# Kernel tuning notes

Measured on AMD Instinct MI355X. Metric: run time of the kernel, lower is better.

The kernel has to match this reference:

```python
import jax, jax.numpy as jnp
import numpy as np

B, S, D = 1, 4096, 768
H = 12
HD = D // H  # 64


def setup_inputs() -> dict:
    key = jax.random.key(0)
    ks = jax.random.split(key, 6)
    sc = 1.0 / np.sqrt(D)
    return {
        "x": jax.random.normal(ks[0], (B, S, D), dtype=jnp.float32),
        "wq": jax.random.normal(ks[1], (D, D), dtype=jnp.float32) * sc,
        "wk": jax.random.normal(ks[2], (D, D), dtype=jnp.float32) * sc,
        "wv": jax.random.normal(ks[3], (D, D), dtype=jnp.float32) * sc,
        "wo": jax.random.normal(ks[4], (D, D), dtype=jnp.float32) * sc,
        "bo": jax.random.normal(ks[5], (D,), dtype=jnp.float32) * 0.02,
    }


def reference(x, wq, wk, wv, wo, bo):
    b, n, _ = x.shape
    # projections (torch Linear: x @ W.T; here weights stored as (d_in, d_out))
    q = (x @ wq).reshape(b, n, H, HD).transpose(0, 2, 1, 3)  # b h n d
    k = (x @ wk).reshape(b, n, H, HD).transpose(0, 2, 1, 3)
    v = (x @ wv).reshape(b, n, H, HD).transpose(0, 2, 1, 3)
    scores = jnp.einsum("bhqd,bhkd->bhqk", q, k)
    causal = jnp.tril(jnp.ones((n, n), dtype=bool))  # True = keep
    scores = jnp.where(causal, scores, -jnp.inf)
    weights = jax.nn.softmax(scores / np.sqrt(HD), axis=-1)
    ctx = jnp.einsum("bhqk,bhkd->bhqd", weights, v)
    ctx = ctx.transpose(0, 2, 1, 3).reshape(b, n, D)
    return ctx @ wo + bo
```

## Files before the change

kernel.cpp:

```cpp
#include <hip/hip_runtime.h>


typedef short bf16x8 __attribute__((ext_vector_type(8)));
typedef float f32x4 __attribute__((ext_vector_type(4)));
typedef unsigned short u16;

static constexpr int S_LEN = 4096;
static constexpr int DIM   = 768;
static constexpr int NH    = 12;
static constexpr float QSCALE = 0.125f * 1.44269504088896340736f;

__device__ inline u16 f2bf(float f) {
  union { float f; unsigned int u; } v; v.f = f;
  unsigned int r = v.u + 0x7FFFu + ((v.u >> 16) & 1u);
  return (u16)(r >> 16);
}

__device__ inline void gload_lds16(const u16* g, u16* s) {
  __builtin_amdgcn_global_load_lds(
      (const __attribute__((address_space(1))) unsigned int*)g,
      (__attribute__((address_space(3))) unsigned int*)s, 16, 0, 0);
}

__device__ inline bf16x8 packP(f32x4 sA, f32x4 sB, float& ls) {
  const float p0 = __builtin_amdgcn_exp2f(sA[0]);
  const float p1 = __builtin_amdgcn_exp2f(sA[1]);
  const float p2 = __builtin_amdgcn_exp2f(sA[2]);
  const float p3 = __builtin_amdgcn_exp2f(sA[3]);
  const float r0 = __builtin_amdgcn_exp2f(sB[0]);
  const float r1 = __builtin_amdgcn_exp2f(sB[1]);
  const float r2 = __builtin_amdgcn_exp2f(sB[2]);
  const float r3 = __builtin_amdgcn_exp2f(sB[3]);
  ls += (p0 + p1 + p2 + p3) + (r0 + r1 + r2 + r3);
  unsigned a0, a1, b0, b1;
  asm("v_cvt_pk_bf16_f32 %0, %1, %2" : "=v"(a0) : "v"(p0), "v"(p1));
  asm("v_cvt_pk_bf16_f32 %0, %1, %2" : "=v"(a1) : "v"(p2), "v"(p3));
  asm("v_cvt_pk_bf16_f32 %0, %1, %2" : "=v"(b0) : "v"(r0), "v"(r1));
  asm("v_cvt_pk_bf16_f32 %0, %1, %2" : "=v"(b1) : "v"(r2), "v"(r3));
  asm("v_permlane32_swap_b32 %0, %1" : "+v"(a0), "+v"(b0));
  asm("v_permlane16_swap_b32 %0, %1" : "+v"(a0), "+v"(b0));
  asm("v_permlane32_swap_b32 %0, %1" : "+v"(a1), "+v"(b1));
  asm("v_permlane16_swap_b32 %0, %1" : "+v"(a1), "+v"(b1));
  union { unsigned u[4]; bf16x8 v; } U;
  U.u[0] = a0; U.u[1] = a1; U.u[2] = b0; U.u[3] = b1;
  return U.v;
}

__device__ inline bf16x8 packPmask(f32x4 sA, f32x4 sB, float& ls,
                                   int kvb, int quad, int qg) {
  float p0 = __builtin_amdgcn_exp2f(sA[0]);
  float p1 = __builtin_amdgcn_exp2f(sA[1]);
  float p2 = __builtin_amdgcn_exp2f(sA[2]);
  float p3 = __builtin_amdgcn_exp2f(sA[3]);
  float r0 = __builtin_amdgcn_exp2f(sB[0]);
  float r1 = __builtin_amdgcn_exp2f(sB[1]);
  float r2 = __builtin_amdgcn_exp2f(sB[2]);
  float r3 = __builtin_amdgcn_exp2f(sB[3]);
  const int k0 = kvb + quad * 4;
  if (k0 + 0 > qg)  p0 = 0.f;
  if (k0 + 1 > qg)  p1 = 0.f;
  if (k0 + 2 > qg)  p2 = 0.f;
  if (k0 + 3 > qg)  p3 = 0.f;
  if (k0 + 16 > qg) r0 = 0.f;
  if (k0 + 17 > qg) r1 = 0.f;
  if (k0 + 18 > qg) r2 = 0.f;
  if (k0 + 19 > qg) r3 = 0.f;
  ls += (p0 + p1 + p2 + p3) + (r0 + r1 + r2 + r3);
  unsigned a0, a1, b0, b1;
  asm("v_cvt_pk_bf16_f32 %0, %1, %2" : "=v"(a0) : "v"(p0), "v"(p1));
  asm("v_cvt_pk_bf16_f32 %0, %1, %2" : "=v"(a1) : "v"(p2), "v"(p3));
  asm("v_cvt_pk_bf16_f32 %0, %1, %2" : "=v"(b0) : "v"(r0), "v"(r1));
  asm("v_cvt_pk_bf16_f32 %0, %1, %2" : "=v"(b1) : "v"(r2), "v"(r3));
  asm("v_permlane32_swap_b32 %0, %1" : "+v"(a0), "+v"(b0));
  asm("v_permlane16_swap_b32 %0, %1" : "+v"(a0), "+v"(b0));
  asm("v_permlane32_swap_b32 %0, %1" : "+v"(a1), "+v"(b1));
  asm("v_permlane16_swap_b32 %0, %1" : "+v"(a1), "+v"(b1));
  union { unsigned u[4]; bf16x8 v; } U;
  U.u[0] = a0; U.u[1] = a1; U.u[2] = b0; U.u[3] = b1;
  return U.v;
}

__global__ __launch_bounds__(256)
void prep_kernel(const float* __restrict__ x, const float* __restrict__ w0,
                 const float* __restrict__ w1, const float* __restrict__ w2,
                 const float* __restrict__ w3, u16* __restrict__ xb,
                 u16* __restrict__ t0, u16* __restrict__ t1,
                 u16* __restrict__ t2, u16* __restrict__ t3) {
  if (blockIdx.z == 4) {
    const size_t n = (size_t)S_LEN * DIM;
    const int id = blockIdx.y * 12 + blockIdx.x;
    const size_t stride = (size_t)144 * 256 * 8;
    for (size_t i = ((size_t)id * 256 + threadIdx.x) * 8; i < n; i += stride) {
      const float4 a = *(const float4*)(x + i);
      const float4 b = *(const float4*)(x + i + 4);
      bf16x8 o;
      o[0] = (short)f2bf(a.x); o[1] = (short)f2bf(a.y);
      o[2] = (short)f2bf(a.z); o[3] = (short)f2bf(a.w);
      o[4] = (short)f2bf(b.x); o[5] = (short)f2bf(b.y);
      o[6] = (short)f2bf(b.z); o[7] = (short)f2bf(b.w);
      *(bf16x8*)(xb + i) = o;
    }
    return;
  }
  __shared__ float T[64][65];
  const float* src; u16* dst;
  switch (blockIdx.z) {
    case 0: src = w0; dst = t0; break;
    case 1: src = w1; dst = t1; break;
    case 2: src = w2; dst = t2; break;
    default: src = w3; dst = t3; break;
  }
  const int k0 = blockIdx.y * 64, n0 = blockIdx.x * 64;
  const int r = threadIdx.x >> 2, c0 = (threadIdx.x & 3) * 16;
#pragma unroll
  for (int i = 0; i < 4; ++i) {
    const float4 v = *(const float4*)(src + (size_t)(k0 + r) * DIM + n0 + c0 + i * 4);
    T[r][c0 + i * 4 + 0] = v.x;
    T[r][c0 + i * 4 + 1] = v.y;
    T[r][c0 + i * 4 + 2] = v.z;
    T[r][c0 + i * 4 + 3] = v.w;
  }
  __syncthreads();
  bf16x8 o0, o1;
#pragma unroll
  for (int i = 0; i < 8; ++i) {
    o0[i] = (short)f2bf(T[c0 + i][r]);
    o1[i] = (short)f2bf(T[c0 + 8 + i][r]);
  }
  *(bf16x8*)(dst + (size_t)(n0 + r) * DIM + k0 + c0) = o0;
  *(bf16x8*)(dst + (size_t)(n0 + r) * DIM + k0 + c0 + 8) = o1;
}

template <int MODE>
__global__ __launch_bounds__(256)
void mfma_gemm_kernel(const u16* __restrict__ A, const u16* __restrict__ Bq,
                      const u16* __restrict__ Bk, const u16* __restrict__ Bv,
                      const float* __restrict__ bias, u16* __restrict__ Qb,
                      u16* __restrict__ Kb, u16* __restrict__ VT,
                      float* __restrict__ Out) {
  constexpr int MT = (MODE == 0) ? 4 : 2;
  constexpr int BM = MT * 32;
  __shared__ __align__(16) u16 Al[BM * 64];
  __shared__ __align__(16) u16 Bl[96 * 64];

  const int tid  = threadIdx.x;
  const int wv   = tid >> 6;
  const int lane = tid & 63;
  const int quad = lane >> 4;
  const int l16  = lane & 15;
  const int wr = wv >> 1, wc = wv & 1;
  const int m0 = blockIdx.y * BM;
  const int n0 = blockIdx.x * 96;

  int wi = 0, nb = n0;
  const u16* BT = Bq;
  if (MODE == 0) {
    wi = n0 / DIM;
    nb = n0 - wi * DIM;
    BT = (wi == 0) ? Bq : (wi == 1) ? Bk : Bv;
  }

  const int sr8 = lane >> 3;
  const int sc  = ((lane & 7) ^ sr8) * 8;
  const int key = l16 & 7;

  const bool swp = (MODE == 1) || (wi < 2);

  f32x4 acc[MT][3] = {};

  for (int k0 = 0; k0 < DIM; k0 += 64) {
    __syncthreads();
#pragma unroll
    for (int j = 0; j < MT; ++j)
      gload_lds16(A + (size_t)(m0 + wv * (BM / 4) + j * 8 + sr8) * DIM + k0 + sc,
                  &Al[(wv * (BM / 4) + j * 8) * 64]);
#pragma unroll
    for (int j = 0; j < 3; ++j)
      gload_lds16(BT + (size_t)(nb + wv * 24 + j * 8 + sr8) * DIM + k0 + sc,
                  &Bl[(wv * 24 + j * 8) * 64]);
    __syncthreads();

#pragma unroll
    for (int kh = 0; kh < 2; ++kh) {
      const int cb = kh * 4;
      bf16x8 af[MT], bfr[3];
#pragma unroll
      for (int mt = 0; mt < MT; ++mt) {
        const int row = wr * (BM / 2) + mt * 16 + l16;
        af[mt] = *(const bf16x8*)&Al[row * 64 + ((cb + quad) ^ key) * 8];
      }
#pragma unroll
      for (int nt = 0; nt < 3; ++nt) {
        const int row = wc * 48 + nt * 16 + l16;
        bfr[nt] = *(const bf16x8*)&Bl[row * 64 + ((cb + quad) ^ key) * 8];
      }
      if (swp) {
#pragma unroll
        for (int mt = 0; mt < MT; ++mt)
#pragma unroll
          for (int nt = 0; nt < 3; ++nt)
            acc[mt][nt] = __builtin_amdgcn_mfma_f32_16x16x32_bf16(
                bfr[nt], af[mt], acc[mt][nt], 0, 0, 0);
      } else {
#pragma unroll
        for (int mt = 0; mt < MT; ++mt)
#pragma unroll
          for (int nt = 0; nt < 3; ++nt)
            acc[mt][nt] = __builtin_amdgcn_mfma_f32_16x16x32_bf16(
                af[mt], bfr[nt], acc[mt][nt], 0, 0, 0);
      }
    }
  }

  if (MODE == 0 && wi >= 2) {
#pragma unroll
    for (int mt = 0; mt < MT; ++mt) {
#pragma unroll
      for (int nt = 0; nt < 3; ++nt) {
        const int row  = m0 + wr * (BM / 2) + mt * 16 + quad * 4;
        const int ncol = nb + wc * 48 + nt * 16 + l16;
        u16 pk[4];
#pragma unroll
        for (int r = 0; r < 4; ++r) pk[r] = f2bf(acc[mt][nt][r]);
        unsigned long long v;
        __builtin_memcpy(&v, pk, 8);
        *(unsigned long long*)(VT + (size_t)ncol * S_LEN + row) = v;
      }
    }
  } else if (MODE == 0) {
    u16* dst = (wi == 0) ? Qb : Kb;
    const float sc_out = (wi == 0) ? QSCALE : 1.0f;
#pragma unroll
    for (int mt = 0; mt < MT; ++mt) {
#pragma unroll
      for (int nt = 0; nt < 3; ++nt) {
        const int row = m0 + wr * (BM / 2) + mt * 16 + l16;
        const int ncb = nb + wc * 48 + nt * 16 + quad * 4;
        u16 pk[4];
#pragma unroll
        for (int r = 0; r < 4; ++r) pk[r] = f2bf(acc[mt][nt][r] * sc_out);
        unsigned long long v;
        __builtin_memcpy(&v, pk, 8);
        *(unsigned long long*)(dst + (size_t)row * DIM + ncb) = v;
      }
    }
  } else {
#pragma unroll
    for (int mt = 0; mt < MT; ++mt) {
#pragma unroll
      for (int nt = 0; nt < 3; ++nt) {
        const int row = m0 + wr * (BM / 2) + mt * 16 + l16;
        const int ncb = n0 + wc * 48 + nt * 16 + quad * 4;
        const float4 b4 = *(const float4*)(bias + ncb);
        float4 ov;
        ov.x = acc[mt][nt][0] + b4.x;
        ov.y = acc[mt][nt][1] + b4.y;
        ov.z = acc[mt][nt][2] + b4.z;
        ov.w = acc[mt][nt][3] + b4.w;
        *(float4*)(Out + (size_t)row * DIM + ncb) = ov;
      }
    }
  }
}

__global__ __launch_bounds__(256, 4)
void attn_mfma_kernel(const u16* __restrict__ Qb, const u16* __restrict__ Kb,
                      const u16* __restrict__ VTb, u16* __restrict__ ctx) {
  __shared__ __align__(16) u16 KVl[128 * 64 + 64 * 128];
  u16* const Kl = KVl;
  u16* const Vl = KVl + 128 * 64;

  const int tid  = threadIdx.x;
  const int w    = tid >> 6;
  const int lane = tid & 63;
  const int quad = lane >> 4;
  const int l16  = lane & 15;
  const int key  = l16 & 7;

  const int id = blockIdx.x;
  const int to = id / 12;
  const int h  = id - to * 12;
  const int qt = 127 - to;
  const int q0 = qt * 32;

  const int sr8  = lane >> 3;
  const int scK  = ((lane & 7) ^ sr8) * 8;
  const int sr16 = lane >> 4;

  bf16x8 aq00, aq01, aq10, aq11;
  {
    const u16* qp0 = Qb + (size_t)(q0 + l16) * DIM + h * 64 + quad * 8;
    aq00 = *(const bf16x8*)(qp0);
    aq01 = *(const bf16x8*)(qp0 + 32);
    const u16* qp1 = Qb + (size_t)(q0 + 16 + l16) * DIM + h * 64 + quad * 8;
    aq10 = *(const bf16x8*)(qp1);
    aq11 = *(const bf16x8*)(qp1 + 32);
  }

  f32x4 o00 = {}, o01 = {}, o02 = {}, o03 = {};
  f32x4 o10 = {}, o11 = {}, o12 = {}, o13 = {};
  float ls0 = 0.f, ls1 = 0.f;
  const int qg0 = q0 + l16;
  const int qg1 = q0 + 16 + l16;

  const int niter = qt / 4 + 1;

#pragma unroll 1
  for (int i = 0; i < niter; ++i) {
    const int k0g = i * 128;
    asm volatile("s_waitcnt lgkmcnt(0)" ::: "memory");
    __builtin_amdgcn_s_barrier();

#pragma unroll
    for (int jj = 0; jj < 4; ++jj)
      gload_lds16(Kb + (size_t)(k0g + w * 32 + jj * 8 + sr8) * DIM + h * 64 + scK,
                  &Kl[(w * 32 + jj * 8) * 64]);
#pragma unroll
    for (int jj = 0; jj < 4; ++jj) {
      const int vrow = w * 16 + jj * 4 + sr16;
      const int vcol = (l16 ^ (vrow & 7)) * 8;
      gload_lds16(VTb + (size_t)(h * 64 + vrow) * S_LEN + k0g + vcol,
                  &Vl[(w * 16 + jj * 4) * 128]);
    }
    asm volatile("s_waitcnt vmcnt(4)" ::: "memory");
    __builtin_amdgcn_s_barrier();

    const int g = 4 * i + w;
    const bool act = g <= qt;
    bf16x8 pa0v, pa1v;
    if (act) {
      __builtin_amdgcn_s_setprio(1);
      const int rA = (w * 32 + l16) * 64;
      const int rB = (w * 32 + 16 + l16) * 64;
      const bf16x8 bk00 = *(const bf16x8*)&Kl[rA + (quad ^ key) * 8];
      const bf16x8 bk01 = *(const bf16x8*)&Kl[rA + ((quad ^ 4) ^ key) * 8];
      const bf16x8 bk10 = *(const bf16x8*)&Kl[rB + (quad ^ key) * 8];
      const bf16x8 bk11 = *(const bf16x8*)&Kl[rB + ((quad ^ 4) ^ key) * 8];
      const f32x4 Z = {0.f, 0.f, 0.f, 0.f};
      f32x4 sA = __builtin_amdgcn_mfma_f32_16x16x32_bf16(bk00, aq00, Z, 0, 0, 0);
      sA = __builtin_amdgcn_mfma_f32_16x16x32_bf16(bk01, aq01, sA, 0, 0, 0);
      f32x4 sB = __builtin_amdgcn_mfma_f32_16x16x32_bf16(bk10, aq00, Z, 0, 0, 0);
      sB = __builtin_amdgcn_mfma_f32_16x16x32_bf16(bk11, aq01, sB, 0, 0, 0);
      f32x4 sC = __builtin_amdgcn_mfma_f32_16x16x32_bf16(bk00, aq10, Z, 0, 0, 0);
      sC = __builtin_amdgcn_mfma_f32_16x16x32_bf16(bk01, aq11, sC, 0, 0, 0);
      f32x4 sD = __builtin_amdgcn_mfma_f32_16x16x32_bf16(bk10, aq10, Z, 0, 0, 0);
      sD = __builtin_amdgcn_mfma_f32_16x16x32_bf16(bk11, aq11, sD, 0, 0, 0);

      if (g == qt) {
        const int kvb = k0g + w * 32;
        pa0v = packPmask(sA, sB, ls0, kvb, quad, qg0);
        pa1v = packPmask(sC, sD, ls1, kvb, quad, qg1);
      } else {
        pa0v = packP(sA, sB, ls0);
        pa1v = packP(sC, sD, ls1);
      }
    }

    asm volatile("s_waitcnt vmcnt(0)" ::: "memory");
    __builtin_amdgcn_s_barrier();

    if (act) {
      const int cc = ((w * 4 + quad) ^ key) * 8;
      const bf16x8 vb0 = *(const bf16x8*)&Vl[(l16) * 128 + cc];
      o00 = __builtin_amdgcn_mfma_f32_16x16x32_bf16(pa0v, vb0, o00, 0, 0, 0);
      o10 = __builtin_amdgcn_mfma_f32_16x16x32_bf16(pa1v, vb0, o10, 0, 0, 0);
      const bf16x8 vb1 = *(const bf16x8*)&Vl[(16 + l16) * 128 + cc];
      o01 = __builtin_amdgcn_mfma_f32_16x16x32_bf16(pa0v, vb1, o01, 0, 0, 0);
      o11 = __builtin_amdgcn_mfma_f32_16x16x32_bf16(pa1v, vb1, o11, 0, 0, 0);
      const bf16x8 vb2 = *(const bf16x8*)&Vl[(32 + l16) * 128 + cc];
      o02 = __builtin_amdgcn_mfma_f32_16x16x32_bf16(pa0v, vb2, o02, 0, 0, 0);
      o12 = __builtin_amdgcn_mfma_f32_16x16x32_bf16(pa1v, vb2, o12, 0, 0, 0);
      const bf16x8 vb3 = *(const bf16x8*)&Vl[(48 + l16) * 128 + cc];
      o03 = __builtin_amdgcn_mfma_f32_16x16x32_bf16(pa0v, vb3, o03, 0, 0, 0);
      o13 = __builtin_amdgcn_mfma_f32_16x16x32_bf16(pa1v, vb3, o13, 0, 0, 0);
      __builtin_amdgcn_s_setprio(0);
    }
  }

  __syncthreads();
  float* Obuf  = (float*)KVl;
  float* lbufF = Obuf + 5120;
  const int bme = (w * 64 + lane) * 20;

  *(f32x4*)&Obuf[bme + 0]  = o00;
  *(f32x4*)&Obuf[bme + 4]  = o01;
  *(f32x4*)&Obuf[bme + 8]  = o02;
  *(f32x4*)&Obuf[bme + 12] = o03;
  lbufF[w * 64 + lane] = ls0;
  __syncthreads();
  if (w == 0) {
#pragma unroll
    for (int wq = 1; wq < 4; ++wq) {
      const int bp = (wq * 64 + lane) * 20;
      o00 += *(const f32x4*)&Obuf[bp + 0];
      o01 += *(const f32x4*)&Obuf[bp + 4];
      o02 += *(const f32x4*)&Obuf[bp + 8];
      o03 += *(const f32x4*)&Obuf[bp + 12];
      ls0 += lbufF[wq * 64 + lane];
    }
  }
  __syncthreads();

  *(f32x4*)&Obuf[bme + 0]  = o10;
  *(f32x4*)&Obuf[bme + 4]  = o11;
  *(f32x4*)&Obuf[bme + 8]  = o12;
  *(f32x4*)&Obuf[bme + 12] = o13;
  lbufF[w * 64 + lane] = ls1;
  __syncthreads();
  if (w == 1) {
#pragma unroll
    for (int wq = 0; wq < 4; ++wq) {
      if (wq == 1) continue;
      const int bp = (wq * 64 + lane) * 20;
      o10 += *(const f32x4*)&Obuf[bp + 0];
      o11 += *(const f32x4*)&Obuf[bp + 4];
      o12 += *(const f32x4*)&Obuf[bp + 8];
      o13 += *(const f32x4*)&Obuf[bp + 12];
      ls1 += lbufF[wq * 64 + lane];
    }
  }

  if (w == 0) {
    float L = ls0;
    L += __shfl_xor(L, 16);
    L += __shfl_xor(L, 32);
#pragma unroll
    for (int r = 0; r < 4; ++r) {
      const float inv = 1.f / __shfl(L, quad * 4 + r);
      const int row = q0 + quad * 4 + r;
      u16* cp = ctx + (size_t)row * DIM + h * 64 + l16;
      cp[0]  = f2bf(o00[r] * inv);
      cp[16] = f2bf(o01[r] * inv);
      cp[32] = f2bf(o02[r] * inv);
      cp[48] = f2bf(o03[r] * inv);
    }
  } else if (w == 1) {
    float L = ls1;
    L += __shfl_xor(L, 16);
    L += __shfl_xor(L, 32);
#pragma unroll
    for (int r = 0; r < 4; ++r) {
      const float inv = 1.f / __shfl(L, quad * 4 + r);
      const int row = q0 + 16 + quad * 4 + r;
      u16* cp = ctx + (size_t)row * DIM + h * 64 + l16;
      cp[0]  = f2bf(o10[r] * inv);
      cp[16] = f2bf(o11[r] * inv);
      cp[32] = f2bf(o12[r] * inv);
      cp[48] = f2bf(o13[r] * inv);
    }
  }
}

extern "C" void kernel_launch(void* const* d_in, const int* in_sizes, int n_in,
                              void* d_out, int out_size, void* d_ws,
                              size_t ws_size, hipStream_t stream) {
  const float* x  = (const float*)d_in[0];
  const float* wq = (const float*)d_in[1];
  const float* wk = (const float*)d_in[2];
  const float* wv = (const float*)d_in[3];
  const float* wo = (const float*)d_in[4];
  const float* bo = (const float*)d_in[5];

  const size_t n_x = (size_t)S_LEN * DIM;
  const size_t n_w = (size_t)DIM * DIM;
  u16* xb  = (u16*)d_ws;
  u16* wtq = xb + n_x;
  u16* wtk = wtq + n_w;
  u16* wtv = wtk + n_w;
  u16* wto = wtv + n_w;
  u16* Qb  = wto + n_w;
  u16* Kb  = Qb + n_x;
  u16* VTb = Kb + n_x;
  u16* ctx = VTb + n_x;

  prep_kernel<<<dim3(12, 12, 5), 256, 0, stream>>>(
      x, wq, wk, wv, wo, xb, wtq, wtk, wtv, wto);

  mfma_gemm_kernel<0><<<dim3(24, 32), 256, 0, stream>>>(
      xb, wtq, wtk, wtv, nullptr, Qb, Kb, VTb, nullptr);

  attn_mfma_kernel<<<dim3(1536), 256, 0, stream>>>(Qb, Kb, VTb, ctx);

  mfma_gemm_kernel<1><<<dim3(8, 64), 256, 0, stream>>>(
      ctx, wto, nullptr, nullptr, bo, nullptr, nullptr, nullptr, (float*)d_out);
}
```

Measured before the change: 156.6 us.

## Double-buffer LDS tiles in projection GEMM to overlap global loads with MFMA

The projection and output GEMM kernel now keeps two LDS buffers for the A and B tiles and prefetches the next k-slice via global_load_lds while the current slice is consumed. Explicit vmcnt waits let only the current tile's loads complete before each barrier. The aim is to hide global memory latency behind MFMA work. In exchange, LDS usage per block doubles, which may reduce occupancy, and correctness now depends on hand-counted vmcnt values.

```diff
diff --git a/kernel.cpp b/kernel.cpp
--- a/kernel.cpp
+++ b/kernel.cpp
@@ -138,10 +138,12 @@
                       const float* __restrict__ bias, u16* __restrict__ Qb,
                       u16* __restrict__ Kb, u16* __restrict__ VT,
                       float* __restrict__ Out) {
-  constexpr int MT = (MODE == 0) ? 4 : 2;
-  constexpr int BM = MT * 32;
-  __shared__ __align__(16) u16 Al[BM * 64];
-  __shared__ __align__(16) u16 Bl[96 * 64];
+  constexpr int MT  = (MODE == 0) ? 4 : 2;
+  constexpr int BM  = MT * 32;
+  constexpr int ASZ = BM * 64;
+  constexpr int BSZ = 96 * 64;
+  __shared__ __align__(16) u16 Al[2 * ASZ];
+  __shared__ __align__(16) u16 Bl[2 * BSZ];
 
   const int tid  = threadIdx.x;
   const int wv   = tid >> 6;
@@ -168,17 +170,39 @@
 
   f32x4 acc[MT][3] = {};
 
-  for (int k0 = 0; k0 < DIM; k0 += 64) {
-    __syncthreads();
-#pragma unroll
-    for (int j = 0; j < MT; ++j)
-      gload_lds16(A + (size_t)(m0 + wv * (BM / 4) + j * 8 + sr8) * DIM + k0 + sc,
-                  &Al[(wv * (BM / 4) + j * 8) * 64]);
-#pragma unroll
-    for (int j = 0; j < 3; ++j)
-      gload_lds16(BT + (size_t)(nb + wv * 24 + j * 8 + sr8) * DIM + k0 + sc,
-                  &Bl[(wv * 24 + j * 8) * 64]);
-    __syncthreads();
+  constexpr int NK = DIM / 64;
+
+#pragma unroll
+  for (int j = 0; j < MT; ++j)
+    gload_lds16(A + (size_t)(m0 + wv * (BM / 4) + j * 8 + sr8) * DIM + sc,
+                &Al[(wv * (BM / 4) + j * 8) * 64]);
+#pragma unroll
+  for (int j = 0; j < 3; ++j)
+    gload_lds16(BT + (size_t)(nb + wv * 24 + j * 8 + sr8) * DIM + sc,
+                &Bl[(wv * 24 + j * 8) * 64]);
+
+  for (int k = 0; k < NK; ++k) {
+    asm volatile("s_waitcnt lgkmcnt(0)" ::: "memory");
+    __builtin_amdgcn_s_barrier();
+
+    const int cur = k & 1;
+    if (k + 1 < NK) {
+      const int nxt = (k + 1) & 1;
+      const int k0n = (k + 1) * 64;
+#pragma unroll
+      for (int j = 0; j < MT; ++j)
+        gload_lds16(A + (size_t)(m0 + wv * (BM / 4) + j * 8 + sr8) * DIM + k0n + sc,
+                    &Al[nxt * ASZ + (wv * (BM / 4) + j * 8) * 64]);
+#pragma unroll
+      for (int j = 0; j < 3; ++j)
+        gload_lds16(BT + (size_t)(nb + wv * 24 + j * 8 + sr8) * DIM + k0n + sc,
+                    &Bl[nxt * BSZ + (wv * 24 + j * 8) * 64]);
+      if (MODE == 0) asm volatile("s_waitcnt vmcnt(7)" ::: "memory");
+      else           asm volatile("s_waitcnt vmcnt(5)" ::: "memory");
+    } else {
+      asm volatile("s_waitcnt vmcnt(0)" ::: "memory");
+    }
+    __builtin_amdgcn_s_barrier();
 
 #pragma unroll
     for (int kh = 0; kh < 2; ++kh) {
@@ -187,12 +211,12 @@
 #pragma unroll
       for (int mt = 0; mt < MT; ++mt) {
         const int row = wr * (BM / 2) + mt * 16 + l16;
-        af[mt] = *(const bf16x8*)&Al[row * 64 + ((cb + quad) ^ key) * 8];
+        af[mt] = *(const bf16x8*)&Al[cur * ASZ + row * 64 + ((cb + quad) ^ key) * 8];
       }
 #pragma unroll
       for (int nt = 0; nt < 3; ++nt) {
         const int row = wc * 48 + nt * 16 + l16;
-        bfr[nt] = *(const bf16x8*)&Bl[row * 64 + ((cb + quad) ^ key) * 8];
+        bfr[nt] = *(const bf16x8*)&Bl[cur * BSZ + row * 64 + ((cb + quad) ^ key) * 8];
       }
       if (swp) {
 #pragma unroll
```

Result: slower. 164.4 us (+5.0%).
